# Kernel optimization log

Measured on AMD Instinct MI355X. Metric: run time of the kernel, lower is better.

## Reference

```python
import jax, jax.numpy as jnp
import numpy as np

SCALE_BASE = 512.0
GAMMA = 0.96875


def _rotate_every_two(x):
    x1 = x[..., ::2]
    x2 = x[..., 1::2]
    return jnp.stack([-x2, x1], axis=-1).reshape(x.shape)


def _dup_interleave(m):
    # [L, d/2] -> [L, d], each column duplicated: (a,b) -> (a,a,b,b)
    return jnp.repeat(m, 2, axis=-1)


def _xpos(x, downscale=False):
    # x: [B, L, d]; offset = 0 (parallel form)
    B, L, d = x.shape
    half = d // 2
    pos = jnp.arange(L, dtype=x.dtype)
    # xpos per-channel scale base
    sv = (jnp.arange(0, d, 2, dtype=x.dtype) + 0.4 * d) / (1.4 * d)   # [d/2]
    scale = sv[None, :] ** (pos[:, None] / SCALE_BASE)                 # [L, d/2]
    if downscale:
        scale = 1.0 / scale
    inv_freq = 1.0 / (10000.0 ** (jnp.arange(half, dtype=x.dtype) / half))
    sinusoid = pos[:, None] * inv_freq[None, :]                        # [L, d/2]
    sin = _dup_interleave(jnp.sin(sinusoid) * scale)                   # [L, d]
    cos = _dup_interleave(jnp.cos(sinusoid) * scale)                   # [L, d]
    return x * cos[None] + _rotate_every_two(x) * sin[None]


def _get_D(seq_len, dtype):
    idx = jnp.arange(seq_len)
    diff = idx[:, None] - idx[None, :]                                 # n - m
    safe = jnp.where(diff >= 0, diff, 0).astype(dtype)
    return jnp.where(diff >= 0, GAMMA ** safe, jnp.zeros((), dtype))   # [L, L]


def setup_inputs() -> dict:
    key = jax.random.key(0)
    k1, k2, k3, k4 = jax.random.split(key, 4)
    B, L, H, D = 2, 4096, 1024, 64
    X = jax.random.normal(k1, (B, L, H), dtype=jnp.float32)
    W_Q = jax.random.normal(k2, (H, D), dtype=jnp.float32) / H
    W_K = jax.random.normal(k3, (H, D), dtype=jnp.float32) / H
    W_V = jax.random.normal(k4, (H, D), dtype=jnp.float32) / H
    return {"X": X, "W_Q": W_Q, "W_K": W_K, "W_V": W_V}


def reference(X, W_Q, W_K, W_V):
    L = X.shape[1]
    Dmask = _get_D(L, X.dtype)                     # [L, L]
    Q = _xpos(X @ W_Q)                             # [B, L, d]
    K = _xpos(X @ W_K, downscale=True)             # [B, L, d]
    V = X @ W_V                                    # [B, L, v]
    ret = jnp.einsum('bnd,bmd->bnm', Q, K) * Dmask[None]  # [B, L, L]
    return ret @ V                                 # [B, L, v]
```

## Files before the change

### kernel.cpp

```cpp
#include <hip/hip_runtime.h>
#include <math.h>

#define NB 2
#define LL 4096
#define HH 1024
#define DD 64
#define CHK 64
#define NCH 64
#define BLROWS (NB*LL)
#define NCHT (NB*NCH)
#define GAMMA 0.96875f

typedef _Float16 f16x8 __attribute__((ext_vector_type(8)));
typedef _Float16 f16x4 __attribute__((ext_vector_type(4)));
typedef float    f32x4 __attribute__((ext_vector_type(4)));

#define WCH 12288

__global__ __launch_bounds__(256) void prep_w(
    const float* __restrict__ WQ, const float* __restrict__ WK,
    const float* __restrict__ WV, _Float16* __restrict__ Whg,
    _Float16* __restrict__ Wlg)
{
    const unsigned t = blockIdx.x * 256 + threadIdx.x;
    const unsigned kchunk = t / 1536u;
    const unsigned s = t - kchunk * 1536u;
    const int ct2  = s >> 6;
    const int lane = s & 63;
    const int n16  = ct2 >> 1;
    const int kt   = ct2 & 1;
    const int quad = lane >> 4;
    const int n    = n16 * 16 + (lane & 15);
    const int k0   = (int)kchunk * 64 + kt * 32 + quad * 8;
    const int m    = n >> 6;
    const int d    = n & 63;
    const float* Wm = (m == 0) ? WQ : (m == 1) ? WK : WV;
    f16x8 hv, lv;
#pragma unroll
    for (int j = 0; j < 8; ++j) {
        const float x = Wm[(size_t)(k0 + j) * DD + d] * 1024.f;
        const _Float16 h = (_Float16)x;
        hv[j] = h;
        lv[j] = (_Float16)(x - (float)h);
    }
    *(f16x8*)&Whg[(size_t)t * 8] = hv;
    *(f16x8*)&Wlg[(size_t)t * 8] = lv;
}

__global__ __launch_bounds__(256) void proj_mfma(
    const float* __restrict__ X, const _Float16* __restrict__ Whg,
    const _Float16* __restrict__ Wlg, _Float16* __restrict__ Qr,
    _Float16* __restrict__ Kr, _Float16* __restrict__ Vr)
{
    __shared__ __align__(16) _Float16 lds[12288];
    _Float16* Xh = lds;
    _Float16* Xl = lds + 2048;
    _Float16* Wh = lds + 4096;
    _Float16* Wl = lds + 8192;

    const int tid  = threadIdx.x;
    const int wv   = tid >> 6;
    const int lane = tid & 63;
    const int quad = lane >> 4;
    const int l15  = lane & 15;
    const int r0   = (blockIdx.x & 255) * 32;
    const int cb4  = (blockIdx.x >> 8) * 4;
    const int rt   = wv & 1;
    const int cp   = (wv >> 1) * 2;

    const int xrow = tid >> 3;
    const int xk8  = (tid & 7) * 8;
    const int xslot = (((xrow >> 4) * 2 + (xk8 >> 5)) * 64 +
                       ((xk8 >> 3) & 3) * 16 + (xrow & 15)) * 8;

    f32x4 acc[2];
    acc[0] = (f32x4){0.f, 0.f, 0.f, 0.f};
    acc[1] = (f32x4){0.f, 0.f, 0.f, 0.f};

    float4 pxa, pxb;
    f16x8  pwh[2], pwl2[2];
    {
        const float* xp = &X[(size_t)(r0 + xrow) * HH + xk8];
        pxa = *(const float4*)&xp[0];
        pxb = *(const float4*)&xp[4];
#pragma unroll
        for (int i = 0; i < 2; ++i) {
            const int s = tid + i * 256;
            const int ctl = s >> 7, kt = (s >> 6) & 1, ln = s & 63;
            const size_t off = (size_t)(((cb4 + ctl) * 2 + kt) * 64 + ln) * 8;
            pwh[i]  = *(const f16x8*)&Whg[off];
            pwl2[i] = *(const f16x8*)&Wlg[off];
        }
    }

    for (int ch = 0; ch < 16; ++ch) {
        __syncthreads();
        {
            const float xv[8] = {pxa.x, pxa.y, pxa.z, pxa.w,
                                 pxb.x, pxb.y, pxb.z, pxb.w};
            f16x8 hv, lv;
#pragma unroll
            for (int e = 0; e < 8; ++e) {
                const _Float16 h = (_Float16)xv[e];
                hv[e] = h;
                lv[e] = (_Float16)(xv[e] - (float)h);
            }
            *(f16x8*)&Xh[xslot] = hv;
            *(f16x8*)&Xl[xslot] = lv;
#pragma unroll
            for (int i = 0; i < 2; ++i) {
                *(f16x8*)&Wh[(tid + i * 256) * 8] = pwh[i];
                *(f16x8*)&Wl[(tid + i * 256) * 8] = pwl2[i];
            }
        }
        __syncthreads();
        if (ch + 1 < 16) {
            const float* xp = &X[(size_t)(r0 + xrow) * HH + (ch + 1) * 64 + xk8];
            pxa = *(const float4*)&xp[0];
            pxb = *(const float4*)&xp[4];
            const size_t cb = (size_t)(ch + 1) * WCH;
#pragma unroll
            for (int i = 0; i < 2; ++i) {
                const int s = tid + i * 256;
                const int ctl = s >> 7, kt = (s >> 6) & 1, ln = s & 63;
                const size_t off = cb +
                    (size_t)(((cb4 + ctl) * 2 + kt) * 64 + ln) * 8;
                pwh[i]  = *(const f16x8*)&Whg[off];
                pwl2[i] = *(const f16x8*)&Wlg[off];
            }
        }
#pragma unroll
        for (int kt = 0; kt < 2; ++kt) {
            const f16x8 aH = *(const f16x8*)&Xh[((rt * 2 + kt) * 64 + lane) * 8];
            const f16x8 aL = *(const f16x8*)&Xl[((rt * 2 + kt) * 64 + lane) * 8];
#pragma unroll
            for (int cj = 0; cj < 2; ++cj) {
                const int ctl = cp + cj;
                const f16x8 bh = *(const f16x8*)&Wh[((ctl * 2 + kt) * 64 + lane) * 8];
                const f16x8 bl = *(const f16x8*)&Wl[((ctl * 2 + kt) * 64 + lane) * 8];
                acc[cj] = __builtin_amdgcn_mfma_f32_16x16x32_f16(aH, bh, acc[cj], 0, 0, 0);
                acc[cj] = __builtin_amdgcn_mfma_f32_16x16x32_f16(aH, bl, acc[cj], 0, 0, 0);
                acc[cj] = __builtin_amdgcn_mfma_f32_16x16x32_f16(aL, bh, acc[cj], 0, 0, 0);
            }
        }
    }

#pragma unroll
    for (int cj = 0; cj < 2; ++cj) {
        const int ctg = cb4 + cp + cj;
        const f32x4 v = acc[cj];
        const int col = ctg * 16 + l15;
        const int mat = ctg >> 2;
        const int d   = col & 63;
        if (mat < 2) {
            const int i2 = d >> 1;
            const float sv   = (2.f * (float)i2 + 25.6f) / 89.6f;
            const float l2sv = log2f(sv);
            const float ifr  = exp2f(-13.28771237954945f * ((float)i2 / 32.f));
            const float sgn  = (mat == 0) ? 1.f : -1.f;
            _Float16* dst = (mat == 0) ? Qr : Kr;
#pragma unroll
            for (int r = 0; r < 4; ++r) {
                const int row = r0 + rt * 16 + quad * 4 + r;
                const float val = v[r] * (1.f / 1024.f);
                const float p = __shfl_xor(val, 1, 64);
                const float pf  = (float)(row & (LL - 1));
                const float pfs = (float)(row & 63);
                const float scl = exp2f(sgn * (pfs * (1.f / 512.f)) * l2sv);
                float s, c;
                sincosf(pf * ifr, &s, &c);
                s *= scl; c *= scl;
                const float o = ((col & 1) == 0) ? val * c - p * s
                                                 : val * c + p * s;
                dst[(size_t)row * DD + d] = (_Float16)o;
            }
        } else {
#pragma unroll
            for (int r = 0; r < 4; ++r) {
                const int row = r0 + rt * 16 + quad * 4 + r;
                Vr[(size_t)row * DD + d] = (_Float16)(v[r] * (1.f / 1024.f));
            }
        }
    }
}

__global__ __launch_bounds__(256) void chunk_kv(
    const _Float16* __restrict__ Kr, const _Float16* __restrict__ Vr,
    float* __restrict__ U)
{
    __shared__ _Float16 Kl[64 * 64];
    __shared__ _Float16 Vl[64 * 32];
    __shared__ float pwd[64];
    const int tid   = threadIdx.x;
    const int bc    = blockIdx.x;
    const int chunk = bc >> 1;
    const int dph   = (bc & 1) * 32;
    const size_t rbase = (size_t)chunk * CHK * DD;
    const float l2g = log2f(GAMMA);

    if (tid < 64) pwd[tid] = exp2f((float)(63 - tid) * l2g);
    {
        const int row = tid >> 2;
        const int c0  = (tid & 3) * 16;
        *(f16x8*)&Kl[row * 64 + c0]     = *(const f16x8*)&Kr[rbase + (size_t)row * DD + c0];
        *(f16x8*)&Kl[row * 64 + c0 + 8] = *(const f16x8*)&Kr[rbase + (size_t)row * DD + c0 + 8];
        const int c1 = (tid & 3) * 8;
        *(f16x8*)&Vl[row * 32 + c1] = *(const f16x8*)&Vr[rbase + (size_t)row * DD + dph + c1];
    }
    __syncthreads();
    const int dgr = tid >> 4;
    const int dc  = tid & 15;
    float a[4][2] = {{0,0},{0,0},{0,0},{0,0}};
#pragma unroll 8
    for (int j = 0; j < CHK; ++j) {
        const f16x4 kh = *(const f16x4*)&Kl[j * 64 + dgr * 4];
        const float w  = pwd[j];
        const float v0 = (float)Vl[j * 32 + dc * 2]     * w;
        const float v1 = (float)Vl[j * 32 + dc * 2 + 1] * w;
        const float k0 = (float)kh[0], k1 = (float)kh[1];
        const float k2 = (float)kh[2], k3 = (float)kh[3];
        a[0][0] += k0 * v0; a[0][1] += k0 * v1;
        a[1][0] += k1 * v0; a[1][1] += k1 * v1;
        a[2][0] += k2 * v0; a[2][1] += k2 * v1;
        a[3][0] += k3 * v0; a[3][1] += k3 * v1;
    }
#pragma unroll
    for (int r = 0; r < 4; ++r) {
        *(float2*)&U[((size_t)chunk * DD + dgr * 4 + r) * DD + dph + dc * 2] =
            make_float2(a[r][0], a[r][1]);
    }
}

__global__ __launch_bounds__(256) void chunk_out(
    const _Float16* __restrict__ Qr, const _Float16* __restrict__ Kr,
    const _Float16* __restrict__ Vr, const float* __restrict__ U,
    float* __restrict__ out)
{
    __shared__ __align__(16) unsigned char smraw[35648];
    _Float16* Sb  = (_Float16*)smraw;
    _Float16* Vl  = (_Float16*)(smraw + 8704);
    float*    Tl  = (float*)(smraw + 17920);
    float*    pwl = (float*)(smraw + 35328);

    const int tid   = threadIdx.x;
    const int bc    = blockIdx.x;
    const int chunk = bc >> 1;
    const int nh    = (bc & 1) * 32;
    const int w     = tid >> 6;
    const int lane  = tid & 63;
    const int quad  = lane >> 4;
    const int l15   = lane & 15;
    const int mtile = w >> 1;
    const int npair = (w & 1) * 2;
    const size_t rowbase = (size_t)chunk * CHK + nh;
    const float l2g = log2f(GAMMA);

    if (tid < 65) pwl[tid] = exp2f((float)tid * l2g);

    {
        const int row = tid >> 2;
        const int c0  = (tid & 3) * 16;
        const size_t rb = (size_t)chunk * CHK * DD;
        *(f16x8*)&Vl[row * 72 + c0]     = *(const f16x8*)&Vr[rb + (size_t)row * DD + c0];
        *(f16x8*)&Vl[row * 72 + c0 + 8] = *(const f16x8*)&Vr[rb + (size_t)row * DD + c0 + 8];
    }
    {
        const int d  = tid >> 2;
        const int dq = (tid & 3) * 16;
        const int cloc = chunk & 63;
        const float sv = (2.f * (float)(d >> 1) + 25.6f) / 89.6f;
        const float l2sv = log2f(sv);
        float acc[16];
#pragma unroll
        for (int i = 0; i < 16; ++i) acc[i] = 0.f;
        for (int dl = 1; dl <= 8; ++dl) {
            if (dl <= cloc) {
                const float f = exp2f(64.f * (float)(dl - 1) * l2g +
                                      0.125f * (float)dl * l2sv);
                const float* up = &U[((size_t)(chunk - dl) * DD + d) * DD + dq];
#pragma unroll
                for (int i4 = 0; i4 < 4; ++i4) {
                    const float4 u = *(const float4*)&up[i4 * 4];
                    acc[i4 * 4 + 0] += f * u.x; acc[i4 * 4 + 1] += f * u.y;
                    acc[i4 * 4 + 2] += f * u.z; acc[i4 * 4 + 3] += f * u.w;
                }
            }
        }
#pragma unroll
        for (int i = 0; i < 16; ++i) Tl[d * 68 + dq + i] = acc[i];
    }

    f16x8 aQ[2], bK[2][2];
#pragma unroll
    for (int ks = 0; ks < 2; ++ks)
        aQ[ks] = *(const f16x8*)&Qr[(rowbase + mtile * 16 + l15) * DD +
                                    ks * 32 + quad * 8];
#pragma unroll
    for (int nt = 0; nt < 2; ++nt)
#pragma unroll
        for (int ks = 0; ks < 2; ++ks)
            bK[nt][ks] = *(const f16x8*)&Kr[((size_t)chunk * CHK +
                                            (npair + nt) * 16 + l15) * DD +
                                            ks * 32 + quad * 8];
    __syncthreads();

    f32x4 sA[2] = {(f32x4){0.f,0.f,0.f,0.f}, (f32x4){0.f,0.f,0.f,0.f}};
#pragma unroll
    for (int nt = 0; nt < 2; ++nt)
#pragma unroll
        for (int ks = 0; ks < 2; ++ks)
            sA[nt] = __builtin_amdgcn_mfma_f32_16x16x32_f16(aQ[ks], bK[nt][ks],
                                                            sA[nt], 0, 0, 0);
#pragma unroll
    for (int nt = 0; nt < 2; ++nt) {
        const int m = (npair + nt) * 16 + l15;
#pragma unroll
        for (int r = 0; r < 4; ++r) {
            const int nl = mtile * 16 + quad * 4 + r;
            const int n64 = nh + nl;
            const float val = (n64 >= m) ? sA[nt][r] * pwl[n64 - m] : 0.f;
            Sb[nl * 136 + m] = (_Float16)val;
        }
    }
    if ((w & 1) == 0) {
        const float g = pwl[nh + mtile * 16 + l15 + 1];
#pragma unroll
        for (int ks = 0; ks < 2; ++ks) {
            f16x8 qv;
#pragma unroll
            for (int j = 0; j < 8; ++j)
                qv[j] = (_Float16)((float)aQ[ks][j] * g);
            *(f16x8*)&Sb[(mtile * 16 + l15) * 136 + 64 + ks * 32 + quad * 8] = qv;
        }
    }
    __syncthreads();

    f32x4 oA[2] = {(f32x4){0.f,0.f,0.f,0.f}, (f32x4){0.f,0.f,0.f,0.f}};
#pragma unroll
    for (int ks = 0; ks < 4; ++ks) {
        const f16x8 aS = *(const f16x8*)&Sb[(mtile * 16 + l15) * 136 +
                                            ks * 32 + quad * 8];
#pragma unroll
        for (int nt = 0; nt < 2; ++nt) {
            const int dp = (npair + nt) * 16 + l15;
            f16x8 bV;
            if (ks < 2) {
#pragma unroll
                for (int j = 0; j < 8; ++j)
                    bV[j] = Vl[(ks * 32 + quad * 8 + j) * 72 + dp];
            } else {
#pragma unroll
                for (int j = 0; j < 8; ++j)
                    bV[j] = (_Float16)Tl[((ks - 2) * 32 + quad * 8 + j) * 68 + dp];
            }
            oA[nt] = __builtin_amdgcn_mfma_f32_16x16x32_f16(aS, bV, oA[nt], 0, 0, 0);
        }
    }
#pragma unroll
    for (int nt = 0; nt < 2; ++nt)
#pragma unroll
        for (int r = 0; r < 4; ++r)
            out[(rowbase + mtile * 16 + quad * 4 + r) * DD +
                (npair + nt) * 16 + l15] = oA[nt][r];
}

extern "C" void kernel_launch(void* const* d_in, const int* in_sizes, int n_in,
                              void* d_out, int out_size, void* d_ws, size_t ws_size,
                              hipStream_t stream)
{
    const float* X  = (const float*)d_in[0];
    const float* WQ = (const float*)d_in[1];
    const float* WK = (const float*)d_in[2];
    const float* WV = (const float*)d_in[3];
    float* outp = (float*)d_out;

    _Float16* Whg = (_Float16*)d_ws;
    _Float16* Wlg = Whg + 196608;
    _Float16* Qr  = Wlg + 196608;
    _Float16* Kr  = Qr + (size_t)BLROWS * DD;
    _Float16* Vr  = Kr + (size_t)BLROWS * DD;
    float*    U   = (float*)(Vr + (size_t)BLROWS * DD);

    hipLaunchKernelGGL(prep_w, dim3(96), dim3(256), 0, stream,
                       WQ, WK, WV, Whg, Wlg);
    hipLaunchKernelGGL(proj_mfma, dim3(768), dim3(256), 0, stream,
                       X, Whg, Wlg, Qr, Kr, Vr);
    hipLaunchKernelGGL(chunk_kv, dim3(2 * NCHT), dim3(256), 0, stream, Kr, Vr, U);
    hipLaunchKernelGGL(chunk_out, dim3(2 * NCHT), dim3(256), 0, stream,
                       Qr, Kr, Vr, U, outp);
}
```

Baseline: 113.1 us.

## Replace chunked state recurrence with direct 8-chunk windowed attention; drop prep and kv kernels

Removes the prep_w and chunk_kv kernels. The W hi/lo fp16 split is now done inside the projection kernel, and the chunk_out kernel computes the decayed scores directly against the previous 8 chunks of K (rescaled by gamma and the xpos factor) instead of reading summed U states. K and V are written in fragment-friendly interleaved layouts so the MFMA operands load as 16-byte vectors from global memory. This saves two launches and the U intermediate, but each output block does about 9x more QK and SV MFMA work. The 8-chunk window also truncates contributions where the decay is negligible, as the previous code already did.

```diff
diff --git a/kernel.cpp b/kernel.cpp
--- a/kernel.cpp
+++ b/kernel.cpp
@@ -15,42 +15,11 @@
 typedef _Float16 f16x4 __attribute__((ext_vector_type(4)));
 typedef float    f32x4 __attribute__((ext_vector_type(4)));
 
-#define WCH 12288
-
-__global__ __launch_bounds__(256) void prep_w(
-    const float* __restrict__ WQ, const float* __restrict__ WK,
-    const float* __restrict__ WV, _Float16* __restrict__ Whg,
-    _Float16* __restrict__ Wlg)
-{
-    const unsigned t = blockIdx.x * 256 + threadIdx.x;
-    const unsigned kchunk = t / 1536u;
-    const unsigned s = t - kchunk * 1536u;
-    const int ct2  = s >> 6;
-    const int lane = s & 63;
-    const int n16  = ct2 >> 1;
-    const int kt   = ct2 & 1;
-    const int quad = lane >> 4;
-    const int n    = n16 * 16 + (lane & 15);
-    const int k0   = (int)kchunk * 64 + kt * 32 + quad * 8;
-    const int m    = n >> 6;
-    const int d    = n & 63;
-    const float* Wm = (m == 0) ? WQ : (m == 1) ? WK : WV;
-    f16x8 hv, lv;
-#pragma unroll
-    for (int j = 0; j < 8; ++j) {
-        const float x = Wm[(size_t)(k0 + j) * DD + d] * 1024.f;
-        const _Float16 h = (_Float16)x;
-        hv[j] = h;
-        lv[j] = (_Float16)(x - (float)h);
-    }
-    *(f16x8*)&Whg[(size_t)t * 8] = hv;
-    *(f16x8*)&Wlg[(size_t)t * 8] = lv;
-}
-
 __global__ __launch_bounds__(256) void proj_mfma(
-    const float* __restrict__ X, const _Float16* __restrict__ Whg,
-    const _Float16* __restrict__ Wlg, _Float16* __restrict__ Qr,
-    _Float16* __restrict__ Kr, _Float16* __restrict__ Vr)
+    const float* __restrict__ X, const float* __restrict__ WQ,
+    const float* __restrict__ WK, const float* __restrict__ WV,
+    _Float16* __restrict__ Qr, _Float16* __restrict__ Kf,
+    _Float16* __restrict__ Vf)
 {
     __shared__ __align__(16) _Float16 lds[12288];
     _Float16* Xh = lds;
@@ -67,30 +36,35 @@
     const int cb4  = (blockIdx.x >> 8) * 4;
     const int rt   = wv & 1;
     const int cp   = (wv >> 1) * 2;
+    const float* Wm = (cb4 == 0) ? WQ : (cb4 == 4) ? WK : WV;
 
     const int xrow = tid >> 3;
     const int xk8  = (tid & 7) * 8;
     const int xslot = (((xrow >> 4) * 2 + (xk8 >> 5)) * 64 +
                        ((xk8 >> 3) & 3) * 16 + (xrow & 15)) * 8;
+    int wd[2], wk[2];
+#pragma unroll
+    for (int i = 0; i < 2; ++i) {
+        const int s = tid + i * 256;
+        wd[i] = (s >> 7) * 16 + (s & 15);
+        wk[i] = ((s >> 6) & 1) * 32 + ((s >> 4) & 3) * 8;
+    }
 
     f32x4 acc[2];
     acc[0] = (f32x4){0.f, 0.f, 0.f, 0.f};
     acc[1] = (f32x4){0.f, 0.f, 0.f, 0.f};
 
     float4 pxa, pxb;
-    f16x8  pwh[2], pwl2[2];
+    float  pw[2][8];
     {
         const float* xp = &X[(size_t)(r0 + xrow) * HH + xk8];
         pxa = *(const float4*)&xp[0];
         pxb = *(const float4*)&xp[4];
 #pragma unroll
-        for (int i = 0; i < 2; ++i) {
-            const int s = tid + i * 256;
-            const int ctl = s >> 7, kt = (s >> 6) & 1, ln = s & 63;
-            const size_t off = (size_t)(((cb4 + ctl) * 2 + kt) * 64 + ln) * 8;
-            pwh[i]  = *(const f16x8*)&Whg[off];
-            pwl2[i] = *(const f16x8*)&Wlg[off];
-        }
+        for (int i = 0; i < 2; ++i)
+#pragma unroll
+            for (int j = 0; j < 8; ++j)
+                pw[i][j] = Wm[(size_t)(wk[i] + j) * DD + wd[i]];
     }
 
     for (int ch = 0; ch < 16; ++ch) {
@@ -109,8 +83,16 @@
             *(f16x8*)&Xl[xslot] = lv;
 #pragma unroll
             for (int i = 0; i < 2; ++i) {
-                *(f16x8*)&Wh[(tid + i * 256) * 8] = pwh[i];
-                *(f16x8*)&Wl[(tid + i * 256) * 8] = pwl2[i];
+                f16x8 whv, wlv;
+#pragma unroll
+                for (int j = 0; j < 8; ++j) {
+                    const float x = pw[i][j] * 1024.f;
+                    const _Float16 h = (_Float16)x;
+                    whv[j] = h;
+                    wlv[j] = (_Float16)(x - (float)h);
+                }
+                *(f16x8*)&Wh[(tid + i * 256) * 8] = whv;
+                *(f16x8*)&Wl[(tid + i * 256) * 8] = wlv;
             }
         }
         __syncthreads();
@@ -118,16 +100,12 @@
             const float* xp = &X[(size_t)(r0 + xrow) * HH + (ch + 1) * 64 + xk8];
             pxa = *(const float4*)&xp[0];
             pxb = *(const float4*)&xp[4];
-            const size_t cb = (size_t)(ch + 1) * WCH;
-#pragma unroll
-            for (int i = 0; i < 2; ++i) {
-                const int s = tid + i * 256;
-                const int ctl = s >> 7, kt = (s >> 6) & 1, ln = s & 63;
-                const size_t off = cb +
-                    (size_t)(((cb4 + ctl) * 2 + kt) * 64 + ln) * 8;
-                pwh[i]  = *(const f16x8*)&Whg[off];
-                pwl2[i] = *(const f16x8*)&Wlg[off];
-            }
+            const int kb = (ch + 1) * 64;
+#pragma unroll
+            for (int i = 0; i < 2; ++i)
+#pragma unroll
+                for (int j = 0; j < 8; ++j)
+                    pw[i][j] = Wm[(size_t)(kb + wk[i] + j) * DD + wd[i]];
         }
 #pragma unroll
         for (int kt = 0; kt < 2; ++kt) {
@@ -158,7 +136,6 @@
             const float l2sv = log2f(sv);
             const float ifr  = exp2f(-13.28771237954945f * ((float)i2 / 32.f));
             const float sgn  = (mat == 0) ? 1.f : -1.f;
-            _Float16* dst = (mat == 0) ? Qr : Kr;
 #pragma unroll
             for (int r = 0; r < 4; ++r) {
                 const int row = r0 + rt * 16 + quad * 4 + r;
@@ -172,75 +149,33 @@
                 s *= scl; c *= scl;
                 const float o = ((col & 1) == 0) ? val * c - p * s
                                                  : val * c + p * s;
-                dst[(size_t)row * DD + d] = (_Float16)o;
+                if (mat == 0) {
+                    Qr[(size_t)row * DD + d] = (_Float16)o;
+                } else {
+                    const int b = row >> 12, posb = row & 4095;
+                    Kf[(((size_t)b * 8 + (d >> 3)) * 4096 + posb) * 8 + (d & 7)] =
+                        (_Float16)o;
+                }
             }
         } else {
-#pragma unroll
-            for (int r = 0; r < 4; ++r) {
-                const int row = r0 + rt * 16 + quad * 4 + r;
-                Vr[(size_t)row * DD + d] = (_Float16)(v[r] * (1.f / 1024.f));
-            }
+            f16x4 vv;
+#pragma unroll
+            for (int r = 0; r < 4; ++r) vv[r] = (_Float16)(v[r] * (1.f / 1024.f));
+            const int row0 = r0 + rt * 16 + quad * 4;
+            const int b = row0 >> 12, posb = row0 & 4095;
+            *(f16x4*)&Vf[(((size_t)b * 512 + (posb >> 3)) * 64 + d) * 8 + (posb & 7)] = vv;
         }
     }
 }
 
-__global__ __launch_bounds__(256) void chunk_kv(
-    const _Float16* __restrict__ Kr, const _Float16* __restrict__ Vr,
-    float* __restrict__ U)
+__global__ __launch_bounds__(256) void chunk_out(
+    const _Float16* __restrict__ Qr, const _Float16* __restrict__ Kf,
+    const _Float16* __restrict__ Vf, float* __restrict__ out)
 {
-    __shared__ _Float16 Kl[64 * 64];
-    __shared__ _Float16 Vl[64 * 32];
-    __shared__ float pwd[64];
-    const int tid   = threadIdx.x;
-    const int bc    = blockIdx.x;
-    const int chunk = bc >> 1;
-    const int dph   = (bc & 1) * 32;
-    const size_t rbase = (size_t)chunk * CHK * DD;
-    const float l2g = log2f(GAMMA);
-
-    if (tid < 64) pwd[tid] = exp2f((float)(63 - tid) * l2g);
-    {
-        const int row = tid >> 2;
-        const int c0  = (tid & 3) * 16;
-        *(f16x8*)&Kl[row * 64 + c0]     = *(const f16x8*)&Kr[rbase + (size_t)row * DD + c0];
-        *(f16x8*)&Kl[row * 64 + c0 + 8] = *(const f16x8*)&Kr[rbase + (size_t)row * DD + c0 + 8];
-        const int c1 = (tid & 3) * 8;
-        *(f16x8*)&Vl[row * 32 + c1] = *(const f16x8*)&Vr[rbase + (size_t)row * DD + dph + c1];
-    }
-    __syncthreads();
-    const int dgr = tid >> 4;
-    const int dc  = tid & 15;
-    float a[4][2] = {{0,0},{0,0},{0,0},{0,0}};
-#pragma unroll 8
-    for (int j = 0; j < CHK; ++j) {
-        const f16x4 kh = *(const f16x4*)&Kl[j * 64 + dgr * 4];
-        const float w  = pwd[j];
-        const float v0 = (float)Vl[j * 32 + dc * 2]     * w;
-        const float v1 = (float)Vl[j * 32 + dc * 2 + 1] * w;
-        const float k0 = (float)kh[0], k1 = (float)kh[1];
-        const float k2 = (float)kh[2], k3 = (float)kh[3];
-        a[0][0] += k0 * v0; a[0][1] += k0 * v1;
-        a[1][0] += k1 * v0; a[1][1] += k1 * v1;
-        a[2][0] += k2 * v0; a[2][1] += k2 * v1;
-        a[3][0] += k3 * v0; a[3][1] += k3 * v1;
-    }
-#pragma unroll
-    for (int r = 0; r < 4; ++r) {
-        *(float2*)&U[((size_t)chunk * DD + dgr * 4 + r) * DD + dph + dc * 2] =
-            make_float2(a[r][0], a[r][1]);
-    }
-}
-
-__global__ __launch_bounds__(256) void chunk_out(
-    const _Float16* __restrict__ Qr, const _Float16* __restrict__ Kr,
-    const _Float16* __restrict__ Vr, const float* __restrict__ U,
-    float* __restrict__ out)
-{
-    __shared__ __align__(16) unsigned char smraw[35648];
+    __shared__ __align__(16) unsigned char smraw[38464];
     _Float16* Sb  = (_Float16*)smraw;
-    _Float16* Vl  = (_Float16*)(smraw + 8704);
-    float*    Tl  = (float*)(smraw + 17920);
-    float*    pwl = (float*)(smraw + 35328);
+    _Float16* svp = (_Float16*)(smraw + 37120);
+    float*    pwl = (float*)(smraw + 38144);
 
     const int tid   = threadIdx.x;
     const int bc    = blockIdx.x;
@@ -250,118 +185,110 @@
     const int lane  = tid & 63;
     const int quad  = lane >> 4;
     const int l15   = lane & 15;
-    const int mtile = w >> 1;
+    const int mt    = w >> 1;
     const int npair = (w & 1) * 2;
+    const int cloc  = chunk & 63;
+    const int bB    = chunk >> 6;
     const size_t rowbase = (size_t)chunk * CHK + nh;
     const float l2g = log2f(GAMMA);
 
     if (tid < 65) pwl[tid] = exp2f((float)tid * l2g);
-
-    {
-        const int row = tid >> 2;
-        const int c0  = (tid & 3) * 16;
-        const size_t rb = (size_t)chunk * CHK * DD;
-        *(f16x8*)&Vl[row * 72 + c0]     = *(const f16x8*)&Vr[rb + (size_t)row * DD + c0];
-        *(f16x8*)&Vl[row * 72 + c0 + 8] = *(const f16x8*)&Vr[rb + (size_t)row * DD + c0 + 8];
-    }
-    {
-        const int d  = tid >> 2;
-        const int dq = (tid & 3) * 16;
-        const int cloc = chunk & 63;
-        const float sv = (2.f * (float)(d >> 1) + 25.6f) / 89.6f;
-        const float l2sv = log2f(sv);
-        float acc[16];
-#pragma unroll
-        for (int i = 0; i < 16; ++i) acc[i] = 0.f;
-        for (int dl = 1; dl <= 8; ++dl) {
-            if (dl <= cloc) {
-                const float f = exp2f(64.f * (float)(dl - 1) * l2g +
-                                      0.125f * (float)dl * l2sv);
-                const float* up = &U[((size_t)(chunk - dl) * DD + d) * DD + dq];
-#pragma unroll
-                for (int i4 = 0; i4 < 4; ++i4) {
-                    const float4 u = *(const float4*)&up[i4 * 4];
-                    acc[i4 * 4 + 0] += f * u.x; acc[i4 * 4 + 1] += f * u.y;
-                    acc[i4 * 4 + 2] += f * u.z; acc[i4 * 4 + 3] += f * u.w;
-                }
-            }
-        }
-#pragma unroll
-        for (int i = 0; i < 16; ++i) Tl[d * 68 + dq + i] = acc[i];
-    }
-
-    f16x8 aQ[2], bK[2][2];
+#pragma unroll
+    for (int e = 0; e < 2; ++e) {
+        const int idx = tid + e * 256;
+        const int dl  = (idx >> 6) + 1;
+        const int dd  = idx & 63;
+        const float sv = (2.f * (float)(dd >> 1) + 25.6f) / 89.6f;
+        svp[idx] = (_Float16)exp2f(0.125f * (float)dl * log2f(sv));
+    }
+
+    f16x8 aQ[2];
 #pragma unroll
     for (int ks = 0; ks < 2; ++ks)
-        aQ[ks] = *(const f16x8*)&Qr[(rowbase + mtile * 16 + l15) * DD +
+        aQ[ks] = *(const f16x8*)&Qr[(rowbase + mt * 16 + l15) * DD +
                                     ks * 32 + quad * 8];
-#pragma unroll
-    for (int nt = 0; nt < 2; ++nt)
-#pragma unroll
-        for (int ks = 0; ks < 2; ++ks)
-            bK[nt][ks] = *(const f16x8*)&Kr[((size_t)chunk * CHK +
-                                            (npair + nt) * 16 + l15) * DD +
-                                            ks * 32 + quad * 8];
     __syncthreads();
 
     f32x4 sA[2] = {(f32x4){0.f,0.f,0.f,0.f}, (f32x4){0.f,0.f,0.f,0.f}};
 #pragma unroll
-    for (int nt = 0; nt < 2; ++nt)
-#pragma unroll
-        for (int ks = 0; ks < 2; ++ks)
-            sA[nt] = __builtin_amdgcn_mfma_f32_16x16x32_f16(aQ[ks], bK[nt][ks],
-                                                            sA[nt], 0, 0, 0);
+    for (int nt = 0; nt < 2; ++nt) {
+        const int posb = cloc * 64 + (npair + nt) * 16 + l15;
+#pragma unroll
+        for (int ks = 0; ks < 2; ++ks) {
+            const f16x8 bK = *(const f16x8*)&Kf[(((size_t)bB * 8 + ks * 4 + quad)
+                                                * 4096 + posb) * 8];
+            sA[nt] = __builtin_amdgcn_mfma_f32_16x16x32_f16(aQ[ks], bK, sA[nt], 0, 0, 0);
+        }
+    }
 #pragma unroll
     for (int nt = 0; nt < 2; ++nt) {
         const int m = (npair + nt) * 16 + l15;
 #pragma unroll
         for (int r = 0; r < 4; ++r) {
-            const int nl = mtile * 16 + quad * 4 + r;
+            const int nl = mt * 16 + quad * 4 + r;
             const int n64 = nh + nl;
             const float val = (n64 >= m) ? sA[nt][r] * pwl[n64 - m] : 0.f;
-            Sb[nl * 136 + m] = (_Float16)val;
-        }
-    }
-    if ((w & 1) == 0) {
-        const float g = pwl[nh + mtile * 16 + l15 + 1];
+            Sb[nl * 580 + m] = (_Float16)val;
+        }
+    }
+
+    for (int jc = (w & 1); jc < 32; jc += 2) {
+        const int dlt = 8 - (jc >> 2);
+        const bool valid = (dlt <= cloc);
+        const int mq = (jc * 16 + l15) & 63;
+        const float gl = valid ? exp2f((float)(64 * dlt - mq) * l2g) : 0.f;
+        const _Float16 glh = (_Float16)gl;
+        const int cs = valid ? (chunk - dlt) : chunk;
+        const int posb = (cs & 63) * 64 + mq;
+        f32x4 sc4 = (f32x4){0.f, 0.f, 0.f, 0.f};
 #pragma unroll
         for (int ks = 0; ks < 2; ++ks) {
-            f16x8 qv;
-#pragma unroll
-            for (int j = 0; j < 8; ++j)
-                qv[j] = (_Float16)((float)aQ[ks][j] * g);
-            *(f16x8*)&Sb[(mtile * 16 + l15) * 136 + 64 + ks * 32 + quad * 8] = qv;
+            const f16x8 bk = *(const f16x8*)&Kf[(((size_t)bB * 8 + ks * 4 + quad)
+                                                * 4096 + posb) * 8];
+            const f16x8 sv8 = *(const f16x8*)&svp[(dlt - 1) * 64 + ks * 32 + quad * 8];
+            f16x8 b2;
+#pragma unroll
+            for (int j = 0; j < 8; ++j) b2[j] = bk[j] * glh * sv8[j];
+            sc4 = __builtin_amdgcn_mfma_f32_16x16x32_f16(aQ[ks], b2, sc4, 0, 0, 0);
+        }
+#pragma unroll
+        for (int r = 0; r < 4; ++r) {
+            const int nl = mt * 16 + quad * 4 + r;
+            const int na = nh + nl;
+            Sb[nl * 580 + 64 + jc * 16 + l15] = (_Float16)(sc4[r] * pwl[na]);
         }
     }
     __syncthreads();
 
     f32x4 oA[2] = {(f32x4){0.f,0.f,0.f,0.f}, (f32x4){0.f,0.f,0.f,0.f}};
-#pragma unroll
-    for (int ks = 0; ks < 4; ++ks) {
-        const f16x8 aS = *(const f16x8*)&Sb[(mtile * 16 + l15) * 136 +
-                                            ks * 32 + quad * 8];
-#pragma unroll
-        for (int nt = 0; nt < 2; ++nt) {
-            const int dp = (npair + nt) * 16 + l15;
-            f16x8 bV;
-            if (ks < 2) {
-#pragma unroll
-                for (int j = 0; j < 8; ++j)
-                    bV[j] = Vl[(ks * 32 + quad * 8 + j) * 72 + dp];
-            } else {
-#pragma unroll
-                for (int j = 0; j < 8; ++j)
-                    bV[j] = (_Float16)Tl[((ks - 2) * 32 + quad * 8 + j) * 68 + dp];
-            }
-            oA[nt] = __builtin_amdgcn_mfma_f32_16x16x32_f16(aS, bV, oA[nt], 0, 0, 0);
-        }
-    }
-#pragma unroll
-    for (int nt = 0; nt < 2; ++nt)
+    for (int ks5 = 0; ks5 < 18; ++ks5) {
+        const f16x8 aS = *(const f16x8*)&Sb[(mt * 16 + l15) * 580 +
+                                            ks5 * 32 + quad * 8];
+        const int m0 = ks5 * 32 + quad * 8;
+        int gr;
+        if (ks5 < 2) {
+            gr = chunk * 64 + m0;
+        } else {
+            const int mc = m0 - 64;
+            int cs2 = chunk - 8 + (mc >> 6);
+            if (cs2 < (chunk & ~63)) cs2 = chunk;
+            gr = cs2 * 64 + (mc & 63);
+        }
+        const int b2 = gr >> 12, pb = gr & 4095;
+        const size_t vb = ((size_t)b2 * 512 + (pb >> 3)) * 64;
+#pragma unroll
+        for (int t = 0; t < 2; ++t) {
+            const int dp = (npair + t) * 16 + l15;
+            const f16x8 bV = *(const f16x8*)&Vf[(vb + dp) * 8];
+            oA[t] = __builtin_amdgcn_mfma_f32_16x16x32_f16(aS, bV, oA[t], 0, 0, 0);
+        }
+    }
+#pragma unroll
+    for (int t = 0; t < 2; ++t)
 #pragma unroll
         for (int r = 0; r < 4; ++r)
-            out[(rowbase + mtile * 16 + quad * 4 + r) * DD +
-                (npair + nt) * 16 + l15] = oA[nt][r];
+            out[(rowbase + mt * 16 + quad * 4 + r) * DD +
+                (npair + t) * 16 + l15] = oA[t][r];
 }
 
 extern "C" void kernel_launch(void* const* d_in, const int* in_sizes, int n_in,
@@ -374,18 +301,12 @@
     const float* WV = (const float*)d_in[3];
     float* outp = (float*)d_out;
 
-    _Float16* Whg = (_Float16*)d_ws;
-    _Float16* Wlg = Whg + 196608;
-    _Float16* Qr  = Wlg + 196608;
-    _Float16* Kr  = Qr + (size_t)BLROWS * DD;
-    _Float16* Vr  = Kr + (size_t)BLROWS * DD;
-    float*    U   = (float*)(Vr + (size_t)BLROWS * DD);
-
-    hipLaunchKernelGGL(prep_w, dim3(96), dim3(256), 0, stream,
-                       WQ, WK, WV, Whg, Wlg);
+    _Float16* Qr = (_Float16*)d_ws;
+    _Float16* Kf = Qr + (size_t)BLROWS * DD;
+    _Float16* Vf = Kf + (size_t)BLROWS * DD;
+
     hipLaunchKernelGGL(proj_mfma, dim3(768), dim3(256), 0, stream,
-                       X, Whg, Wlg, Qr, Kr, Vr);
-    hipLaunchKernelGGL(chunk_kv, dim3(2 * NCHT), dim3(256), 0, stream, Kr, Vr, U);
+                       X, WQ, WK, WV, Qr, Kf, Vf);
     hipLaunchKernelGGL(chunk_out, dim3(2 * NCHT), dim3(256), 0, stream,
-                       Qr, Kr, Vr, U, outp);
+                       Qr, Kf, Vf, outp);
 }
```

Result: no change. 113.3 us (+0.2%).
